# Optimization experiments

Measured on AMD Instinct MI355X. Metric: run time of the kernel, lower is better.

Reference implementation:

```python
import jax, jax.numpy as jnp
import numpy as np

D_MODEL = 1024
D_STATE = 16
D_CONV = 4
EXPAND = 2
D_INNER = EXPAND * D_MODEL  # 2048
DT_RANK = (D_MODEL + 15) // 16  # 64
BATCH = 2
SEQ = 1024


def setup_inputs() -> dict:
    key = jax.random.key(0)
    ks = jax.random.split(key, 9)
    s = 0.02
    x = jax.random.normal(ks[0], (BATCH, SEQ, D_MODEL), jnp.float32)
    W_in = jax.random.normal(ks[1], (D_MODEL, 2 * D_INNER), jnp.float32) * s
    conv_w = jax.random.normal(ks[2], (D_INNER, D_CONV), jnp.float32) * s
    conv_b = jnp.zeros((D_INNER,), jnp.float32)
    W_x = jax.random.normal(ks[3], (D_INNER, DT_RANK + 2 * D_STATE), jnp.float32) * s
    W_dt = jax.random.normal(ks[4], (DT_RANK, D_INNER), jnp.float32) * (DT_RANK ** -0.5)
    # dt bias init: inverse softplus of dt ~ U(1e-3, 0.1)
    dt0 = jax.random.uniform(ks[5], (D_INNER,), jnp.float32, 1e-3, 0.1)
    b_dt = dt0 + jnp.log(-jnp.expm1(-dt0))
    # S4D-real A init: A[d, n] = -(n+1)
    A_log = jnp.log(jnp.tile(jnp.arange(1, D_STATE + 1, dtype=jnp.float32), (D_INNER, 1)))
    D_skip = jnp.ones((D_INNER,), jnp.float32)
    W_out = jax.random.normal(ks[6], (D_INNER, D_MODEL), jnp.float32) * s
    return {"x": x, "W_in": W_in, "conv_w": conv_w, "conv_b": conv_b,
            "W_x": W_x, "W_dt": W_dt, "b_dt": b_dt, "A_log": A_log,
            "D_skip": D_skip, "W_out": W_out}


def _mamba_forward(x, W_in, conv_w, conv_b, W_x, W_dt, b_dt, A_log, D_skip, W_out):
    Bsz, L, _ = x.shape
    # input projection -> [B, L, 2*d_inner], split into stream and gate
    xz = x @ W_in
    xr, z = jnp.split(xz, 2, axis=-1)
    # depthwise causal conv1d over time
    xt = xr.transpose(0, 2, 1)                       # [B, d_inner, L]
    kern = conv_w[:, None, :]                        # [d_inner, 1, d_conv]
    xc = jax.lax.conv_general_dilated(
        xt, kern, window_strides=(1,), padding=[(D_CONV - 1, 0)],
        feature_group_count=D_INNER, dimension_numbers=("NCH", "OIH", "NCH"))
    xc = jax.nn.silu(xc + conv_b[None, :, None]).transpose(0, 2, 1)  # [B, L, d_inner]
    # data-dependent dt, B, C
    dbl = xc @ W_x                                   # [B, L, dt_rank + 2*d_state]
    dt, Bm, Cm = jnp.split(dbl, [DT_RANK, DT_RANK + D_STATE], axis=-1)
    dt = jax.nn.softplus(dt @ W_dt + b_dt)           # [B, L, d_inner]
    A = -jnp.exp(A_log)                              # [d_inner, d_state]

    def step(h, inp):
        dt_t, B_t, C_t, x_t = inp                    # [B,d_inner],[B,d_state],[B,d_state],[B,d_inner]
        dA = jnp.exp(dt_t[..., None] * A)            # [B, d_inner, d_state]
        h = dA * h + (dt_t * x_t)[..., None] * B_t[:, None, :]
        y = jnp.einsum("bds,bs->bd", h, C_t)
        return h, y

    h0 = jnp.zeros((Bsz, D_INNER, D_STATE), x.dtype)
    xs = (dt.transpose(1, 0, 2), Bm.transpose(1, 0, 2),
          Cm.transpose(1, 0, 2), xc.transpose(1, 0, 2))
    _, ys = jax.lax.scan(step, h0, xs)               # ys: [L, B, d_inner]
    y = ys.transpose(1, 0, 2) + xc * D_skip
    y = y * jax.nn.silu(z)
    return y @ W_out                                 # [B, L, d_model]


def reference(x, W_in, conv_w, conv_b, W_x, W_dt, b_dt, A_log, D_skip, W_out):
    return _mamba_forward(x, W_in, conv_w, conv_b, W_x, W_dt, b_dt, A_log, D_skip, W_out)
```

## Files before the change

### kernel.cpp

```cpp
#include <hip/hip_runtime.h>

#define BATCH 2
#define SEQL 1024
#define DMODEL 1024
#define DINNER 2048
#define DSTATE 16
#define DTRANK 64
#define NCH 64
#define LC 16

typedef short bf16x8 __attribute__((ext_vector_type(8)));
typedef float f32x4 __attribute__((ext_vector_type(4)));
typedef int i32x4 __attribute__((ext_vector_type(4)));

__device__ __forceinline__ unsigned short f2bf(float f) {
  unsigned u = __float_as_uint(f);
  return (unsigned short)((u + 0x7fffu + ((u >> 16) & 1u)) >> 16);
}
__device__ __forceinline__ float sigmoidf_(float x) { return 1.f / (1.f + __expf(-x)); }

__device__ __forceinline__ void gl_lds16(const unsigned short* g, unsigned short* l) {
  __builtin_amdgcn_global_load_lds(
      (const __attribute__((address_space(1))) unsigned int*)g,
      (__attribute__((address_space(3))) unsigned int*)l, 16, 0, 0);
}

#define BM 128
#define BN 128

__global__ __launch_bounds__(256) void k_gemm_mfma(
    const unsigned short* __restrict__ A,
    const unsigned short* __restrict__ Bt,
    float* __restrict__ C, int M, int N, int K,
    const float* __restrict__ bias, int mode)
{
  __shared__ __attribute__((aligned(16))) unsigned short As[128 * 64];
  __shared__ __attribute__((aligned(16))) unsigned short Bs[128 * 64];
  const int tid = threadIdx.x;
  const int wave = tid >> 6, lane = tid & 63;
  const int m0 = blockIdx.x * BM, n0 = blockIdx.y * BN;
  const int Kc = K / gridDim.z;
  const int k0beg = blockIdx.z * Kc;
  float* Cz = C + (size_t)blockIdx.z * M * N;
  const int wr = (wave >> 1) * 64, wc = (wave & 1) * 64;
  const int fr = lane & 15;
  const int qw = lane >> 4;

  int srow[4], scol[4];
  #pragma unroll
  for (int i = 0; i < 4; ++i) {
    int off = wave * 4096 + i * 1024 + lane * 16;
    int row = off >> 7;
    int c16 = ((off >> 4) & 7) ^ (row & 7);
    srow[i] = row;
    scol[i] = c16 * 8;
  }

  f32x4 acc[4][4] = {};
  for (int k0 = k0beg; k0 < k0beg + Kc; k0 += 64) {
    #pragma unroll
    for (int i = 0; i < 4; ++i)
      gl_lds16(A + (size_t)(m0 + srow[i]) * K + k0 + scol[i],
               &As[(wave * 4096 + i * 1024) >> 1]);
    #pragma unroll
    for (int i = 0; i < 4; ++i)
      gl_lds16(Bt + (size_t)(n0 + srow[i]) * K + k0 + scol[i],
               &Bs[(wave * 4096 + i * 1024) >> 1]);
    __syncthreads();
    #pragma unroll
    for (int t = 0; t < 2; ++t) {
      bf16x8 af[4], bfv[4];
      #pragma unroll
      for (int i = 0; i < 4; ++i) {
        int row = wr + i * 16 + fr;
        int c16 = (t * 4 + qw) ^ (row & 7);
        af[i] = *(const bf16x8*)&As[row * 64 + c16 * 8];
      }
      #pragma unroll
      for (int j = 0; j < 4; ++j) {
        int row = wc + j * 16 + fr;
        int c16 = (t * 4 + qw) ^ (row & 7);
        bfv[j] = *(const bf16x8*)&Bs[row * 64 + c16 * 8];
      }
      #pragma unroll
      for (int i = 0; i < 4; ++i)
        #pragma unroll
        for (int j = 0; j < 4; ++j)
          acc[i][j] = __builtin_amdgcn_mfma_f32_16x16x32_bf16(af[i], bfv[j], acc[i][j], 0, 0, 0);
    }
    __syncthreads();
  }
  const int rr = qw * 4;
  if (mode == 1) {
    #pragma unroll
    for (int j = 0; j < 4; ++j) {
      float bj = bias[n0 + wc + j * 16 + fr];
      #pragma unroll
      for (int i = 0; i < 4; ++i)
        #pragma unroll
        for (int r = 0; r < 4; ++r) {
          float v = acc[i][j][r] + bj;
          Cz[(size_t)(m0 + wr + i * 16 + rr + r) * N + (n0 + wc + j * 16 + fr)] =
              __logf(1.f + __expf(v));
        }
    }
  } else {
    #pragma unroll
    for (int i = 0; i < 4; ++i)
      #pragma unroll
      for (int j = 0; j < 4; ++j)
        #pragma unroll
        for (int r = 0; r < 4; ++r)
          Cz[(size_t)(m0 + wr + i * 16 + rr + r) * N + (n0 + wc + j * 16 + fr)] = acc[i][j][r];
  }
}

__global__ void k_reduce2(const float* __restrict__ part, float* __restrict__ dbl,
                          unsigned short* __restrict__ dtraw)
{
  int idx = blockIdx.x * 256 + threadIdx.x;
  float s = 0.f;
  #pragma unroll
  for (int z = 0; z < 8; ++z) s += part[(size_t)z * 2048 * 128 + idx];
  dbl[idx] = s;
  int col = idx & 127, rw = idx >> 7;
  if (col < 64) dtraw[rw * 64 + col] = f2bf(s);
}

__global__ void k_reduce5(const float* __restrict__ part, float* __restrict__ out)
{
  int idx = (blockIdx.x * 256 + threadIdx.x) * 4;
  f32x4 a = *(const f32x4*)(part + idx);
  f32x4 b = *(const f32x4*)(part + (size_t)2048 * 1024 + idx);
  *(f32x4*)(out + idx) = a + b;
}

__global__ void k_f32_to_bf16(const float* __restrict__ in, unsigned short* __restrict__ out, int n)
{
  int i = (blockIdx.x * 256 + threadIdx.x) * 4;
  if (i >= n) return;
  float4 v = *(const float4*)(in + i);
  unsigned short tmp[4] = {f2bf(v.x), f2bf(v.y), f2bf(v.z), f2bf(v.w)};
  *(unsigned long long*)(out + i) = *(unsigned long long*)tmp;
}

__global__ __launch_bounds__(256) void k_transpose_bf16(
    const float* __restrict__ src, unsigned short* __restrict__ dst, int R, int C)
{
  __shared__ float t[64][65];
  int bc = blockIdx.x * 64, br = blockIdx.y * 64;
  int tr = threadIdx.x >> 2;
  int tc = (threadIdx.x & 3) * 16;
  #pragma unroll
  for (int i = 0; i < 4; ++i) {
    float4 v = *(const float4*)(src + (size_t)(br + tr) * C + bc + tc + i * 4);
    t[tr][tc + i * 4 + 0] = v.x; t[tr][tc + i * 4 + 1] = v.y;
    t[tr][tc + i * 4 + 2] = v.z; t[tr][tc + i * 4 + 3] = v.w;
  }
  __syncthreads();
  unsigned short tmp[16];
  #pragma unroll
  for (int i = 0; i < 16; ++i) tmp[i] = f2bf(t[tc + i][tr]);
  unsigned short* dp = dst + (size_t)(bc + tr) * R + br + tc;
  *(i32x4*)dp = *(i32x4*)&tmp[0];
  *(i32x4*)(dp + 8) = *(i32x4*)&tmp[8];
}

__global__ void k_wx_pad_t(const float* __restrict__ Wx, unsigned short* __restrict__ out)
{
  int idx = blockIdx.x * 256 + threadIdx.x;
  int k = idx & (DINNER - 1);
  int n = idx >> 11;
  float v = (n < 96) ? Wx[(size_t)k * 96 + n] : 0.f;
  out[idx] = f2bf(v);
}

__global__ void k_conv_silu(const float* __restrict__ xz, const float* __restrict__ cw,
                            const float* __restrict__ cb, float* __restrict__ xc,
                            unsigned short* __restrict__ xcb)
{
  int idx = blockIdx.x * 256 + threadIdx.x;
  int d = idx & (DINNER - 1);
  int bl = idx >> 11;
  int l = bl & (SEQL - 1);
  float s = cb[d];
  #pragma unroll
  for (int k = 0; k < 4; ++k) {
    int ll = l - 3 + k;
    if (ll >= 0) s += xz[(size_t)(bl - 3 + k) * (2 * DINNER) + d] * cw[d * 4 + k];
  }
  float r = s * sigmoidf_(s);
  xc[idx] = r;
  xcb[idx] = f2bf(r);
}

__global__ __launch_bounds__(256) void k_scan_A(
    const float* __restrict__ dtb, const float* __restrict__ xc,
    const float* __restrict__ dbl, const float* __restrict__ Alog,
    float2* __restrict__ hpair)
{
  __shared__ __attribute__((aligned(16))) float bcB[LC][DSTATE];
  int gid = blockIdx.x * 256 + threadIdx.x;
  int d = gid & (DINNER - 1);
  int t = gid >> 11;
  int c = t & (NCH - 1);
  int b = t >> 6;
  const int r0 = b * SEQL + c * LC;
  bcB[threadIdx.x >> 4][threadIdx.x & 15] =
      dbl[(size_t)(r0 + (threadIdx.x >> 4)) * 128 + 64 + (threadIdx.x & 15)];
  float As[DSTATE];
  #pragma unroll
  for (int i = 0; i < 4; ++i) {
    f32x4 a = *(const f32x4*)&Alog[d * DSTATE + i * 4];
    #pragma unroll
    for (int j = 0; j < 4; ++j) As[i * 4 + j] = -__expf(a[j]);
  }
  __syncthreads();
  float h[DSTATE];
  #pragma unroll
  for (int s = 0; s < DSTATE; ++s) h[s] = 0.f;
  float sumdt = 0.f;
  #pragma unroll
  for (int li = 0; li < LC; li += 2) {
    float dt0 = dtb[(size_t)(r0 + li) * DINNER + d];
    float xv0 = xc [(size_t)(r0 + li) * DINNER + d];
    float dt1 = dtb[(size_t)(r0 + li + 1) * DINNER + d];
    float xv1 = xc [(size_t)(r0 + li + 1) * DINNER + d];
    f32x4 B0[4], B1[4];
    #pragma unroll
    for (int i = 0; i < 4; ++i) B0[i] = *(const f32x4*)&bcB[li][i * 4];
    #pragma unroll
    for (int i = 0; i < 4; ++i) B1[i] = *(const f32x4*)&bcB[li + 1][i * 4];
    float dtx0 = dt0 * xv0, dtx1 = dt1 * xv1;
    sumdt += dt0 + dt1;
    const float* Bv0 = (const float*)B0;
    const float* Bv1 = (const float*)B1;
    #pragma unroll
    for (int s = 0; s < DSTATE; ++s) {
      float dA0 = __expf(dt0 * As[s]);
      h[s] = dA0 * h[s] + dtx0 * Bv0[s];
      float dA1 = __expf(dt1 * As[s]);
      h[s] = dA1 * h[s] + dtx1 * Bv1[s];
    }
  }
  size_t base = ((size_t)(b * NCH + c) * DSTATE) * DINNER + d;
  #pragma unroll
  for (int s = 0; s < DSTATE; ++s) {
    float2 v; v.x = h[s]; v.y = __expf(sumdt * As[s]);
    hpair[base + (size_t)s * DINNER] = v;
  }
}

__global__ void k_scan_B(const float2* __restrict__ hpair, float* __restrict__ hin)
{
  int gid = blockIdx.x * 256 + threadIdx.x;
  int d = gid & (DINNER - 1);
  int s = (gid >> 11) & (DSTATE - 1);
  int b = gid >> 15;
  float h = 0.f;
  for (int c0 = 0; c0 < NCH; c0 += 8) {
    float2 v[8];
    #pragma unroll
    for (int i = 0; i < 8; ++i)
      v[i] = hpair[((size_t)(b * NCH + c0 + i) * DSTATE + s) * DINNER + d];
    #pragma unroll
    for (int i = 0; i < 8; ++i) {
      hin[((size_t)(b * NCH + c0 + i) * DSTATE + s) * DINNER + d] = h;
      h = v[i].y * h + v[i].x;
    }
  }
}

__global__ __launch_bounds__(256) void k_scan_C(
    const float* __restrict__ dtb, const float* __restrict__ xc,
    const float* __restrict__ dbl, const float* __restrict__ Alog,
    const float* __restrict__ hin, const float* __restrict__ Dskip,
    const float* __restrict__ xz, unsigned short* __restrict__ yact)
{
  __shared__ __attribute__((aligned(16))) float bc[LC][32];
  int gid = blockIdx.x * 256 + threadIdx.x;
  int d = gid & (DINNER - 1);
  int t = gid >> 11;
  int c = t & (NCH - 1);
  int b = t >> 6;
  const int r0 = b * SEQL + c * LC;
  {
    int step = threadIdx.x >> 4, j = (threadIdx.x & 15) * 2;
    float2 v = *(const float2*)&dbl[(size_t)(r0 + step) * 128 + 64 + j];
    bc[step][j] = v.x; bc[step][j + 1] = v.y;
  }
  float As[DSTATE];
  #pragma unroll
  for (int i = 0; i < 4; ++i) {
    f32x4 a = *(const f32x4*)&Alog[d * DSTATE + i * 4];
    #pragma unroll
    for (int j = 0; j < 4; ++j) As[i * 4 + j] = -__expf(a[j]);
  }
  float h[DSTATE];
  size_t base = ((size_t)(b * NCH + c) * DSTATE) * DINNER + d;
  #pragma unroll
  for (int s = 0; s < DSTATE; ++s) h[s] = hin[base + (size_t)s * DINNER];
  const float dsk = Dskip[d];
  __syncthreads();
  #pragma unroll
  for (int li = 0; li < LC; li += 2) {
    const int r = r0 + li;
    float dt0 = dtb[(size_t)r * DINNER + d];
    float xv0 = xc [(size_t)r * DINNER + d];
    float zv0 = xz [(size_t)r * (2 * DINNER) + DINNER + d];
    float dt1 = dtb[(size_t)(r + 1) * DINNER + d];
    float xv1 = xc [(size_t)(r + 1) * DINNER + d];
    float zv1 = xz [(size_t)(r + 1) * (2 * DINNER) + DINNER + d];
    f32x4 B0[4], C0[4], B1[4], C1[4];
    #pragma unroll
    for (int i = 0; i < 4; ++i) B0[i] = *(const f32x4*)&bc[li][i * 4];
    #pragma unroll
    for (int i = 0; i < 4; ++i) C0[i] = *(const f32x4*)&bc[li][16 + i * 4];
    #pragma unroll
    for (int i = 0; i < 4; ++i) B1[i] = *(const f32x4*)&bc[li + 1][i * 4];
    #pragma unroll
    for (int i = 0; i < 4; ++i) C1[i] = *(const f32x4*)&bc[li + 1][16 + i * 4];
    const float* Bv0 = (const float*)B0; const float* Cv0 = (const float*)C0;
    const float* Bv1 = (const float*)B1; const float* Cv1 = (const float*)C1;
    float dtx0 = dt0 * xv0, dtx1 = dt1 * xv1;
    float y0 = 0.f, y1 = 0.f;
    #pragma unroll
    for (int s = 0; s < DSTATE; ++s) {
      float dA0 = __expf(dt0 * As[s]);
      h[s] = dA0 * h[s] + dtx0 * Bv0[s];
      y0 += h[s] * Cv0[s];
      float dA1 = __expf(dt1 * As[s]);
      h[s] = dA1 * h[s] + dtx1 * Bv1[s];
      y1 += h[s] * Cv1[s];
    }
    y0 += xv0 * dsk;
    y1 += xv1 * dsk;
    float ya0 = y0 * (zv0 * sigmoidf_(zv0));
    float ya1 = y1 * (zv1 * sigmoidf_(zv1));
    yact[(size_t)r * DINNER + d] = f2bf(ya0);
    yact[(size_t)(r + 1) * DINNER + d] = f2bf(ya1);
  }
}

extern "C" void kernel_launch(void* const* d_in, const int* in_sizes, int n_in,
                              void* d_out, int out_size, void* d_ws, size_t ws_size,
                              hipStream_t stream) {
  const float* x     = (const float*)d_in[0];
  const float* Win   = (const float*)d_in[1];
  const float* cw    = (const float*)d_in[2];
  const float* cbias = (const float*)d_in[3];
  const float* Wx    = (const float*)d_in[4];
  const float* Wdt   = (const float*)d_in[5];
  const float* bdt   = (const float*)d_in[6];
  const float* Alog  = (const float*)d_in[7];
  const float* Dsk   = (const float*)d_in[8];
  const float* Wout  = (const float*)d_in[9];
  float* out = (float*)d_out;

  char* ws = (char*)d_ws;
  size_t o = 0;
  auto alloc = [&](size_t bytes) { char* p = ws + o; o += (bytes + 255) & ~(size_t)255; return p; };
  float*          xz    = (float*)         alloc((size_t)2048 * 4096 * 4);
  unsigned short* xbf   = (unsigned short*)alloc((size_t)2048 * 1024 * 2);
  unsigned short* wint  = (unsigned short*)alloc((size_t)4096 * 1024 * 2);
  float*          xc    = (float*)         alloc((size_t)2048 * 2048 * 4);
  unsigned short* xcb   = (unsigned short*)alloc((size_t)2048 * 2048 * 2);
  unsigned short* wxt   = (unsigned short*)alloc((size_t)128  * 2048 * 2);
  float*          dbl   = (float*)         alloc((size_t)2048 * 128  * 4);
  unsigned short* dtraw = (unsigned short*)alloc((size_t)2048 * 64   * 2);
  unsigned short* wdtt  = (unsigned short*)alloc((size_t)2048 * 64   * 2);
  float*          dtbuf = (float*)         alloc((size_t)2048 * 2048 * 4);
  float2*         hpair = (float2*)        alloc((size_t)2 * NCH * DSTATE * DINNER * 8);
  float*          hin   = (float*)         alloc((size_t)2 * NCH * DSTATE * DINNER * 4);
  unsigned short* yact  = (unsigned short*)alloc((size_t)2048 * 2048 * 2);
  unsigned short* woutt = (unsigned short*)alloc((size_t)1024 * 2048 * 2);
  float* part2 = dtbuf;
  float* part5 = dtbuf;
  (void)ws_size; (void)in_sizes; (void)n_in; (void)out_size;

  k_f32_to_bf16<<<2048, 256, 0, stream>>>(x, xbf, 2048 * 1024);
  k_transpose_bf16<<<dim3(64, 16), 256, 0, stream>>>(Win,  wint,  1024, 4096);
  k_transpose_bf16<<<dim3(16, 32), 256, 0, stream>>>(Wout, woutt, 2048, 1024);
  k_transpose_bf16<<<dim3(32, 1),  256, 0, stream>>>(Wdt,  wdtt,  64,   2048);
  k_wx_pad_t<<<1024, 256, 0, stream>>>(Wx, wxt);

  k_gemm_mfma<<<dim3(16, 32, 1), 256, 0, stream>>>(xbf, wint, xz, 2048, 4096, 1024, nullptr, 0);
  k_conv_silu<<<16384, 256, 0, stream>>>(xz, cw, cbias, xc, xcb);
  k_gemm_mfma<<<dim3(16, 1, 8), 256, 0, stream>>>(xcb, wxt, part2, 2048, 128, 2048, nullptr, 0);
  k_reduce2<<<1024, 256, 0, stream>>>(part2, dbl, dtraw);
  k_gemm_mfma<<<dim3(16, 16, 1), 256, 0, stream>>>(dtraw, wdtt, dtbuf, 2048, 2048, 64, bdt, 1);
  k_scan_A<<<1024, 256, 0, stream>>>(dtbuf, xc, dbl, Alog, hpair);
  k_scan_B<<<256, 256, 0, stream>>>(hpair, hin);
  k_scan_C<<<1024, 256, 0, stream>>>(dtbuf, xc, dbl, Alog, hin, Dsk, xz, yact);
  k_gemm_mfma<<<dim3(16, 8, 2), 256, 0, stream>>>(yact, woutt, part5, 2048, 1024, 2048, nullptr, 0);
  k_reduce5<<<2048, 256, 0, stream>>>(part5, out);
}
```

Measured before the change: 166.3 us.

## Merge prep kernels, store dt/xc/z in bf16, raise split-K factors

Folds the five weight/input conversion kernels into one launch, k_prep. The in-projection GEMM now writes the x half as fp32 and the z gate as bf16. dt is stored as bf16 and the fp32 xc buffer is dropped, so the scans read bf16 dt, xc and z, roughly halving scan memory traffic. Split-K goes from 8 to 16 for the x-projection GEMM and from 2 to 4 for the out-projection, which adds more partial-sum traffic to the reductions. Storing dt and xc in bf16 costs some precision in the scan.

Result: faster. 151.5 us (-8.9%).

```diff
diff --git a/kernel.cpp b/kernel.cpp
--- a/kernel.cpp
+++ b/kernel.cpp
@@ -17,6 +17,9 @@
   unsigned u = __float_as_uint(f);
   return (unsigned short)((u + 0x7fffu + ((u >> 16) & 1u)) >> 16);
 }
+__device__ __forceinline__ float bf2f(unsigned short u) {
+  return __uint_as_float((unsigned)u << 16);
+}
 __device__ __forceinline__ float sigmoidf_(float x) { return 1.f / (1.f + __expf(-x)); }
 
 __device__ __forceinline__ void gl_lds16(const unsigned short* g, unsigned short* l) {
@@ -31,8 +34,8 @@
 __global__ __launch_bounds__(256) void k_gemm_mfma(
     const unsigned short* __restrict__ A,
     const unsigned short* __restrict__ Bt,
-    float* __restrict__ C, int M, int N, int K,
-    const float* __restrict__ bias, int mode)
+    float* __restrict__ C, unsigned short* __restrict__ C2,
+    int M, int N, int K, const float* __restrict__ bias, int mode)
 {
   __shared__ __attribute__((aligned(16))) unsigned short As[128 * 64];
   __shared__ __attribute__((aligned(16))) unsigned short Bs[128 * 64];
@@ -100,9 +103,29 @@
         #pragma unroll
         for (int r = 0; r < 4; ++r) {
           float v = acc[i][j][r] + bj;
-          Cz[(size_t)(m0 + wr + i * 16 + rr + r) * N + (n0 + wc + j * 16 + fr)] =
-              __logf(1.f + __expf(v));
+          C2[(size_t)(m0 + wr + i * 16 + rr + r) * N + (n0 + wc + j * 16 + fr)] =
+              f2bf(__logf(1.f + __expf(v)));
         }
+    }
+  } else if (mode == 2) {
+    if (n0 < 2048) {
+      #pragma unroll
+      for (int i = 0; i < 4; ++i)
+        #pragma unroll
+        for (int j = 0; j < 4; ++j)
+          #pragma unroll
+          for (int r = 0; r < 4; ++r)
+            C[(size_t)(m0 + wr + i * 16 + rr + r) * 2048 + (n0 + wc + j * 16 + fr)] =
+                acc[i][j][r];
+    } else {
+      #pragma unroll
+      for (int i = 0; i < 4; ++i)
+        #pragma unroll
+        for (int j = 0; j < 4; ++j)
+          #pragma unroll
+          for (int r = 0; r < 4; ++r)
+            C2[(size_t)(m0 + wr + i * 16 + rr + r) * 2048 + (n0 - 2048 + wc + j * 16 + fr)] =
+                f2bf(acc[i][j][r]);
     }
   } else {
     #pragma unroll
@@ -115,69 +138,65 @@
   }
 }
 
-__global__ void k_reduce2(const float* __restrict__ part, float* __restrict__ dbl,
-                          unsigned short* __restrict__ dtraw)
-{
-  int idx = blockIdx.x * 256 + threadIdx.x;
-  float s = 0.f;
-  #pragma unroll
-  for (int z = 0; z < 8; ++z) s += part[(size_t)z * 2048 * 128 + idx];
-  dbl[idx] = s;
-  int col = idx & 127, rw = idx >> 7;
-  if (col < 64) dtraw[rw * 64 + col] = f2bf(s);
-}
-
-__global__ void k_reduce5(const float* __restrict__ part, float* __restrict__ out)
-{
-  int idx = (blockIdx.x * 256 + threadIdx.x) * 4;
-  f32x4 a = *(const f32x4*)(part + idx);
-  f32x4 b = *(const f32x4*)(part + (size_t)2048 * 1024 + idx);
-  *(f32x4*)(out + idx) = a + b;
-}
-
-__global__ void k_f32_to_bf16(const float* __restrict__ in, unsigned short* __restrict__ out, int n)
-{
-  int i = (blockIdx.x * 256 + threadIdx.x) * 4;
-  if (i >= n) return;
-  float4 v = *(const float4*)(in + i);
-  unsigned short tmp[4] = {f2bf(v.x), f2bf(v.y), f2bf(v.z), f2bf(v.w)};
-  *(unsigned long long*)(out + i) = *(unsigned long long*)tmp;
-}
-
-__global__ __launch_bounds__(256) void k_transpose_bf16(
-    const float* __restrict__ src, unsigned short* __restrict__ dst, int R, int C)
-{
-  __shared__ float t[64][65];
-  int bc = blockIdx.x * 64, br = blockIdx.y * 64;
+__device__ __forceinline__ void transpose_tile(
+    const float* __restrict__ src, unsigned short* __restrict__ dst,
+    int R, int C, int bx, int by, float* t )
+{
+  int bc = bx * 64, br = by * 64;
   int tr = threadIdx.x >> 2;
   int tc = (threadIdx.x & 3) * 16;
   #pragma unroll
   for (int i = 0; i < 4; ++i) {
     float4 v = *(const float4*)(src + (size_t)(br + tr) * C + bc + tc + i * 4);
-    t[tr][tc + i * 4 + 0] = v.x; t[tr][tc + i * 4 + 1] = v.y;
-    t[tr][tc + i * 4 + 2] = v.z; t[tr][tc + i * 4 + 3] = v.w;
+    t[tr * 65 + tc + i * 4 + 0] = v.x; t[tr * 65 + tc + i * 4 + 1] = v.y;
+    t[tr * 65 + tc + i * 4 + 2] = v.z; t[tr * 65 + tc + i * 4 + 3] = v.w;
   }
   __syncthreads();
   unsigned short tmp[16];
   #pragma unroll
-  for (int i = 0; i < 16; ++i) tmp[i] = f2bf(t[tc + i][tr]);
+  for (int i = 0; i < 16; ++i) tmp[i] = f2bf(t[(tc + i) * 65 + tr]);
   unsigned short* dp = dst + (size_t)(bc + tr) * R + br + tc;
   *(i32x4*)dp = *(i32x4*)&tmp[0];
   *(i32x4*)(dp + 8) = *(i32x4*)&tmp[8];
 }
 
-__global__ void k_wx_pad_t(const float* __restrict__ Wx, unsigned short* __restrict__ out)
-{
-  int idx = blockIdx.x * 256 + threadIdx.x;
-  int k = idx & (DINNER - 1);
-  int n = idx >> 11;
-  float v = (n < 96) ? Wx[(size_t)k * 96 + n] : 0.f;
-  out[idx] = f2bf(v);
-}
-
-__global__ void k_conv_silu(const float* __restrict__ xz, const float* __restrict__ cw,
-                            const float* __restrict__ cb, float* __restrict__ xc,
-                            unsigned short* __restrict__ xcb)
+__global__ __launch_bounds__(256) void k_prep(
+    const float* __restrict__ x,   unsigned short* __restrict__ xbf,
+    const float* __restrict__ Win, unsigned short* __restrict__ wint,
+    const float* __restrict__ Wout,unsigned short* __restrict__ woutt,
+    const float* __restrict__ Wdt, unsigned short* __restrict__ wdtt,
+    const float* __restrict__ Wx,  unsigned short* __restrict__ wxt)
+{
+  __shared__ float t[64 * 65];
+  int bid = blockIdx.x;
+  if (bid < 1024) {
+    int i = (bid * 256 + threadIdx.x) * 8;
+    float4 a = *(const float4*)(x + i);
+    float4 b = *(const float4*)(x + i + 4);
+    unsigned short tmp[8] = {f2bf(a.x), f2bf(a.y), f2bf(a.z), f2bf(a.w),
+                             f2bf(b.x), f2bf(b.y), f2bf(b.z), f2bf(b.w)};
+    *(i32x4*)(xbf + i) = *(i32x4*)tmp;
+  } else if (bid < 2048) {
+    int tt = bid - 1024;
+    transpose_tile(Win, wint, 1024, 4096, tt & 63, tt >> 6, t);
+  } else if (bid < 2560) {
+    int tt = bid - 2048;
+    transpose_tile(Wout, woutt, 2048, 1024, tt & 15, tt >> 4, t);
+  } else if (bid < 2592) {
+    int tt = bid - 2560;
+    transpose_tile(Wdt, wdtt, 64, 2048, tt, 0, t);
+  } else {
+    int idx = (bid - 2592) * 256 + threadIdx.x;
+    int k = idx & (DINNER - 1);
+    int n = idx >> 11;
+    float v = (n < 96) ? Wx[(size_t)k * 96 + n] : 0.f;
+    wxt[idx] = f2bf(v);
+  }
+}
+
+__global__ __launch_bounds__(256) void k_conv_silu(
+    const float* __restrict__ xr, const float* __restrict__ cw,
+    const float* __restrict__ cb, unsigned short* __restrict__ xcb)
 {
   int idx = blockIdx.x * 256 + threadIdx.x;
   int d = idx & (DINNER - 1);
@@ -187,15 +206,36 @@
   #pragma unroll
   for (int k = 0; k < 4; ++k) {
     int ll = l - 3 + k;
-    if (ll >= 0) s += xz[(size_t)(bl - 3 + k) * (2 * DINNER) + d] * cw[d * 4 + k];
+    if (ll >= 0) s += xr[(size_t)(bl - 3 + k) * DINNER + d] * cw[d * 4 + k];
   }
   float r = s * sigmoidf_(s);
-  xc[idx] = r;
   xcb[idx] = f2bf(r);
 }
 
+__global__ void k_reduce2(const float* __restrict__ part, float* __restrict__ dbl,
+                          unsigned short* __restrict__ dtraw)
+{
+  int idx = blockIdx.x * 256 + threadIdx.x;
+  float s = 0.f;
+  #pragma unroll
+  for (int z = 0; z < 16; ++z) s += part[(size_t)z * 2048 * 128 + idx];
+  dbl[idx] = s;
+  int col = idx & 127, rw = idx >> 7;
+  if (col < 64) dtraw[rw * 64 + col] = f2bf(s);
+}
+
+__global__ void k_reduce5(const float* __restrict__ part, float* __restrict__ out)
+{
+  int idx = (blockIdx.x * 256 + threadIdx.x) * 4;
+  f32x4 s = *(const f32x4*)(part + idx);
+  #pragma unroll
+  for (int z = 1; z < 4; ++z)
+    s += *(const f32x4*)(part + (size_t)z * 2048 * 1024 + idx);
+  *(f32x4*)(out + idx) = s;
+}
+
 __global__ __launch_bounds__(256) void k_scan_A(
-    const float* __restrict__ dtb, const float* __restrict__ xc,
+    const unsigned short* __restrict__ dtb, const unsigned short* __restrict__ xcb,
     const float* __restrict__ dbl, const float* __restrict__ Alog,
     float2* __restrict__ hpair)
 {
@@ -222,10 +262,10 @@
   float sumdt = 0.f;
   #pragma unroll
   for (int li = 0; li < LC; li += 2) {
-    float dt0 = dtb[(size_t)(r0 + li) * DINNER + d];
-    float xv0 = xc [(size_t)(r0 + li) * DINNER + d];
-    float dt1 = dtb[(size_t)(r0 + li + 1) * DINNER + d];
-    float xv1 = xc [(size_t)(r0 + li + 1) * DINNER + d];
+    float dt0 = bf2f(dtb[(size_t)(r0 + li) * DINNER + d]);
+    float xv0 = bf2f(xcb[(size_t)(r0 + li) * DINNER + d]);
+    float dt1 = bf2f(dtb[(size_t)(r0 + li + 1) * DINNER + d]);
+    float xv1 = bf2f(xcb[(size_t)(r0 + li + 1) * DINNER + d]);
     f32x4 B0[4], B1[4];
     #pragma unroll
     for (int i = 0; i < 4; ++i) B0[i] = *(const f32x4*)&bcB[li][i * 4];
@@ -272,10 +312,10 @@
 }
 
 __global__ __launch_bounds__(256) void k_scan_C(
-    const float* __restrict__ dtb, const float* __restrict__ xc,
+    const unsigned short* __restrict__ dtb, const unsigned short* __restrict__ xcb,
     const float* __restrict__ dbl, const float* __restrict__ Alog,
     const float* __restrict__ hin, const float* __restrict__ Dskip,
-    const float* __restrict__ xz, unsigned short* __restrict__ yact)
+    const unsigned short* __restrict__ zb, unsigned short* __restrict__ yact)
 {
   __shared__ __attribute__((aligned(16))) float bc[LC][32];
   int gid = blockIdx.x * 256 + threadIdx.x;
@@ -305,12 +345,12 @@
   #pragma unroll
   for (int li = 0; li < LC; li += 2) {
     const int r = r0 + li;
-    float dt0 = dtb[(size_t)r * DINNER + d];
-    float xv0 = xc [(size_t)r * DINNER + d];
-    float zv0 = xz [(size_t)r * (2 * DINNER) + DINNER + d];
-    float dt1 = dtb[(size_t)(r + 1) * DINNER + d];
-    float xv1 = xc [(size_t)(r + 1) * DINNER + d];
-    float zv1 = xz [(size_t)(r + 1) * (2 * DINNER) + DINNER + d];
+    float dt0 = bf2f(dtb[(size_t)r * DINNER + d]);
+    float xv0 = bf2f(xcb[(size_t)r * DINNER + d]);
+    float zv0 = bf2f(zb [(size_t)r * DINNER + d]);
+    float dt1 = bf2f(dtb[(size_t)(r + 1) * DINNER + d]);
+    float xv1 = bf2f(xcb[(size_t)(r + 1) * DINNER + d]);
+    float zv1 = bf2f(zb [(size_t)(r + 1) * DINNER + d]);
     f32x4 B0[4], C0[4], B1[4], C1[4];
     #pragma unroll
     for (int i = 0; i < 4; ++i) B0[i] = *(const f32x4*)&bc[li][i * 4];
@@ -358,40 +398,34 @@
   float* out = (float*)d_out;
 
   char* ws = (char*)d_ws;
-  size_t o = 0;
-  auto alloc = [&](size_t bytes) { char* p = ws + o; o += (bytes + 255) & ~(size_t)255; return p; };
-  float*          xz    = (float*)         alloc((size_t)2048 * 4096 * 4);
-  unsigned short* xbf   = (unsigned short*)alloc((size_t)2048 * 1024 * 2);
-  unsigned short* wint  = (unsigned short*)alloc((size_t)4096 * 1024 * 2);
-  float*          xc    = (float*)         alloc((size_t)2048 * 2048 * 4);
-  unsigned short* xcb   = (unsigned short*)alloc((size_t)2048 * 2048 * 2);
-  unsigned short* wxt   = (unsigned short*)alloc((size_t)128  * 2048 * 2);
-  float*          dbl   = (float*)         alloc((size_t)2048 * 128  * 4);
-  unsigned short* dtraw = (unsigned short*)alloc((size_t)2048 * 64   * 2);
-  unsigned short* wdtt  = (unsigned short*)alloc((size_t)2048 * 64   * 2);
-  float*          dtbuf = (float*)         alloc((size_t)2048 * 2048 * 4);
-  float2*         hpair = (float2*)        alloc((size_t)2 * NCH * DSTATE * DINNER * 8);
-  float*          hin   = (float*)         alloc((size_t)2 * NCH * DSTATE * DINNER * 4);
-  unsigned short* yact  = (unsigned short*)alloc((size_t)2048 * 2048 * 2);
-  unsigned short* woutt = (unsigned short*)alloc((size_t)1024 * 2048 * 2);
-  float* part2 = dtbuf;
-  float* part5 = dtbuf;
+  const size_t MB = 1 << 20;
+  float*          xr    = (float*)         (ws);
+  unsigned short* xbf   = (unsigned short*)(ws + 16 * MB);
+  unsigned short* wint  = (unsigned short*)(ws + 20 * MB);
+  unsigned short* xcb   = (unsigned short*)(ws + 28 * MB);
+  unsigned short* wxt   = (unsigned short*)(ws + 36 * MB);
+  float*          dbl   = (float*)         (ws + 37 * MB);
+  unsigned short* dtraw = (unsigned short*)(ws + 38 * MB);
+  unsigned short* wdtt  = (unsigned short*)(ws + 39 * MB);
+  unsigned short* dtb16 = (unsigned short*)(ws + 40 * MB);
+  unsigned short* zb    = (unsigned short*)(ws + 48 * MB);
+  float2*         hpair = (float2*)        (ws + 56 * MB);
+  float*          hin   = (float*)         (ws + 88 * MB);
+  unsigned short* yact  = (unsigned short*)(ws + 104 * MB);
+  unsigned short* woutt = (unsigned short*)(ws + 112 * MB);
+  float* part2 = (float*)(ws);
+  float* part5 = (float*)(ws);
   (void)ws_size; (void)in_sizes; (void)n_in; (void)out_size;
 
-  k_f32_to_bf16<<<2048, 256, 0, stream>>>(x, xbf, 2048 * 1024);
-  k_transpose_bf16<<<dim3(64, 16), 256, 0, stream>>>(Win,  wint,  1024, 4096);
-  k_transpose_bf16<<<dim3(16, 32), 256, 0, stream>>>(Wout, woutt, 2048, 1024);
-  k_transpose_bf16<<<dim3(32, 1),  256, 0, stream>>>(Wdt,  wdtt,  64,   2048);
-  k_wx_pad_t<<<1024, 256, 0, stream>>>(Wx, wxt);
-
-  k_gemm_mfma<<<dim3(16, 32, 1), 256, 0, stream>>>(xbf, wint, xz, 2048, 4096, 1024, nullptr, 0);
-  k_conv_silu<<<16384, 256, 0, stream>>>(xz, cw, cbias, xc, xcb);
-  k_gemm_mfma<<<dim3(16, 1, 8), 256, 0, stream>>>(xcb, wxt, part2, 2048, 128, 2048, nullptr, 0);
+  k_prep<<<3616, 256, 0, stream>>>(x, xbf, Win, wint, Wout, woutt, Wdt, wdtt, Wx, wxt);
+  k_gemm_mfma<<<dim3(16, 32, 1), 256, 0, stream>>>(xbf, wint, xr, zb, 2048, 4096, 1024, nullptr, 2);
+  k_conv_silu<<<16384, 256, 0, stream>>>(xr, cw, cbias, xcb);
+  k_gemm_mfma<<<dim3(16, 1, 16), 256, 0, stream>>>(xcb, wxt, part2, nullptr, 2048, 128, 2048, nullptr, 0);
   k_reduce2<<<1024, 256, 0, stream>>>(part2, dbl, dtraw);
-  k_gemm_mfma<<<dim3(16, 16, 1), 256, 0, stream>>>(dtraw, wdtt, dtbuf, 2048, 2048, 64, bdt, 1);
-  k_scan_A<<<1024, 256, 0, stream>>>(dtbuf, xc, dbl, Alog, hpair);
+  k_gemm_mfma<<<dim3(16, 16, 1), 256, 0, stream>>>(dtraw, wdtt, nullptr, dtb16, 2048, 2048, 64, bdt, 1);
+  k_scan_A<<<1024, 256, 0, stream>>>(dtb16, xcb, dbl, Alog, hpair);
   k_scan_B<<<256, 256, 0, stream>>>(hpair, hin);
-  k_scan_C<<<1024, 256, 0, stream>>>(dtbuf, xc, dbl, Alog, hin, Dsk, xz, yact);
-  k_gemm_mfma<<<dim3(16, 8, 2), 256, 0, stream>>>(yact, woutt, part5, 2048, 1024, 2048, nullptr, 0);
+  k_scan_C<<<1024, 256, 0, stream>>>(dtb16, xcb, dbl, Alog, hin, Dsk, zb, yact);
+  k_gemm_mfma<<<dim3(16, 8, 4), 256, 0, stream>>>(yact, woutt, part5, nullptr, 2048, 1024, 2048, nullptr, 0);
   k_reduce5<<<2048, 256, 0, stream>>>(part5, out);
 }
```
